# Optimization experiments

Hardware: AMD Instinct MI355X
Metric: run time of the kernel (lower is better)

Reference implementation:

```python
import jax, jax.numpy as jnp
import numpy as np

N_NODES = 50000
N_EDGES = 400000
N_GRAPHS = 64
D_IN = 256
D_HID = 256
D_OUT = 16


def _gcn_conv(x, edge_index, W, b):
    """PyG-style GCNConv: h = D^{-1/2}(A+I)D^{-1/2} (x @ W) + b."""
    n = x.shape[0]
    loop = jnp.arange(n)
    src = jnp.concatenate([edge_index[0], loop])  # [E+N]
    dst = jnp.concatenate([edge_index[1], loop])
    deg = jax.ops.segment_sum(jnp.ones_like(dst, x.dtype), dst, num_segments=n)
    dinv = jnp.where(deg > 0, jax.lax.rsqrt(deg), jnp.zeros_like(deg))
    norm = dinv[src] * dinv[dst]  # [E+N]
    h = x @ W  # linear transform first (as PyG does)
    msg = h[src] * norm[:, None]  # gather + scale, [E+N, D]
    out = jax.ops.segment_sum(msg, dst, num_segments=n)  # scatter-add
    return out + b


def setup_inputs() -> dict:
    key = jax.random.key(0)
    ks = jax.random.split(key, 12)
    x = jax.random.normal(ks[0], (N_NODES, D_IN), dtype=jnp.float32)
    edge_index = jax.random.randint(ks[1], (2, N_EDGES), 0, N_NODES, dtype=jnp.int64)
    batch = jnp.sort(jax.random.randint(ks[2], (N_NODES,), 0, N_GRAPHS, dtype=jnp.int64))

    def glorot(k, fan_in, fan_out):
        s = np.sqrt(6.0 / (fan_in + fan_out)).astype(np.float32)
        return jax.random.uniform(k, (fan_in, fan_out), jnp.float32, -s, s)

    return {
        "x": x,
        "edge_index": edge_index,
        "batch": batch,
        "W1": glorot(ks[3], D_IN, D_HID), "b1": jnp.zeros((D_HID,), jnp.float32),
        "W2": glorot(ks[4], D_HID, D_HID), "b2": jnp.zeros((D_HID,), jnp.float32),
        "W3": glorot(ks[5], D_HID, D_HID), "b3": jnp.zeros((D_HID,), jnp.float32),
        "Wfc": glorot(ks[6], D_HID, D_OUT), "bfc": jnp.zeros((D_OUT,), jnp.float32),
    }


def reference(x, edge_index, batch, W1, b1, W2, b2, W3, b3, Wfc, bfc):
    h = jax.nn.relu(_gcn_conv(x, edge_index, W1, b1))
    h = jax.nn.relu(_gcn_conv(h, edge_index, W2, b2))
    h = jax.nn.relu(_gcn_conv(h, edge_index, W3, b3))
    # global_mean_pool over batch ids
    sums = jax.ops.segment_sum(h, batch, num_segments=N_GRAPHS)  # [G, D]
    cnts = jax.ops.segment_sum(jnp.ones_like(batch, h.dtype), batch, num_segments=N_GRAPHS)
    pooled = sums / jnp.maximum(cnts, 1.0)[:, None]
    return pooled @ Wfc + bfc  # [G, D_OUT]
```

## Files before the change

### kernel.cpp

```cpp
#include <hip/hip_runtime.h>

#define NN 50000
#define NE 400000
#define NG 64
#define D 256
#define DOUT 16

typedef __attribute__((ext_vector_type(8))) _Float16 f16x8;
typedef __attribute__((ext_vector_type(8))) unsigned short u16x8;
typedef __attribute__((ext_vector_type(4))) float f32x4;

__device__ __forceinline__ unsigned short f2h(float x) {
    union { _Float16 h; unsigned short u; } v;
    v.h = (_Float16)x;
    return v.u;
}
__device__ __forceinline__ float h2f(unsigned short u) {
    union { _Float16 h; unsigned short u; } v;
    v.u = u;
    return (float)v.h;
}


__global__ void k_init(int* __restrict__ cnt, float* __restrict__ pooled,
                       const int* __restrict__ batch, float* __restrict__ inv_cnt,
                       int n) {
    int i = blockIdx.x * 256 + threadIdx.x;
    if (i < n) cnt[i] = 0;
    if (i < NG * D) pooled[i] = 0.f;
    if (blockIdx.x == 0 && threadIdx.x < NG) {
        int g = threadIdx.x;
        int lo = 0, hi = n;
        while (lo < hi) { int mid = (lo + hi) >> 1; if (batch[mid] < g) lo = mid + 1; else hi = mid; }
        int start = lo;
        hi = n;
        while (lo < hi) { int mid = (lo + hi) >> 1; if (batch[mid] < g + 1) lo = mid + 1; else hi = mid; }
        inv_cnt[g] = 1.f / fmaxf((float)(lo - start), 1.f);
    }
}


__global__ void k_split_count(const float* __restrict__ x, unsigned short* __restrict__ ahi,
                              int total4, int xblocks,
                              const float* __restrict__ W1, short* __restrict__ w1h,
                              const float* __restrict__ W2, short* __restrict__ w2h,
                              const float* __restrict__ W3, short* __restrict__ w3h,
                              const int* __restrict__ eidx, int* __restrict__ cnt, int E) {
    int b = blockIdx.x;
    if (b < xblocks) {
        int i = b * 256 + threadIdx.x;
        if (i >= total4) return;
        float4 v = ((const float4*)x)[i];
        ushort4 h;
        h.x = f2h(v.x);
        h.y = f2h(v.y);
        h.z = f2h(v.z);
        h.w = f2h(v.w);
        ((ushort4*)ahi)[i] = h;
    } else if (b < xblocks + 3 * 256) {
        int wb = b - xblocks;
        int which = wb >> 8;
        int idx = (wb & 255) * 256 + threadIdx.x;
        int nn = idx >> 8, k = idx & 255;
        const float* W = (which == 0) ? W1 : (which == 1) ? W2 : W3;
        short* Wh = (which == 0) ? w1h : (which == 1) ? w2h : w3h;
        Wh[idx] = (short)f2h(W[k * 256 + nn]);
    } else {
        int e = (b - xblocks - 3 * 256) * 256 + threadIdx.x;
        if (e < E) atomicAdd(&cnt[eidx[E + e]], 1);
    }
}

__global__ void k_scan1(const int* __restrict__ cnt, int* __restrict__ excl,
                        int* __restrict__ bsums, float* __restrict__ dinv, int n) {
    __shared__ int sh[256];
    int tid = threadIdx.x;
    int base = blockIdx.x * 1024;
    int v[4]; int tsum = 0;
    for (int j = 0; j < 4; ++j) {
        int i = base + tid * 4 + j;
        v[j] = (i < n) ? cnt[i] : 0;
        if (i < n) dinv[i] = rsqrtf((float)(v[j] + 1));
        tsum += v[j];
    }
    sh[tid] = tsum; __syncthreads();
    for (int d = 1; d < 256; d <<= 1) {
        int t = (tid >= d) ? sh[tid - d] : 0;
        __syncthreads();
        sh[tid] += t;
        __syncthreads();
    }
    int run = sh[tid] - tsum;
    for (int j = 0; j < 4; ++j) {
        int i = base + tid * 4 + j;
        if (i < n) excl[i] = run;
        run += v[j];
    }
    if (tid == 255) bsums[blockIdx.x] = sh[255];
}

__global__ void k_scan3(int* __restrict__ row_ptr, const int* __restrict__ bsums,
                        int* __restrict__ cursor, int n, int E, int nb) {
    __shared__ int off_s;
    int chunk = (int)(blockIdx.x >> 2);
    if (threadIdx.x < 64) {
        int v = ((int)threadIdx.x < nb && (int)threadIdx.x < chunk) ? bsums[threadIdx.x] : 0;
        #pragma unroll
        for (int d = 1; d < 64; d <<= 1) v += __shfl_xor(v, d);
        if (threadIdx.x == 0) off_s = v;
    }
    __syncthreads();
    int off = off_s;
    int i = blockIdx.x * 256 + threadIdx.x;
    if (i < n) {
        int v = row_ptr[i] + off;
        row_ptr[i] = v;
        cursor[i] = v;
    }
    if (i == 0) row_ptr[n] = E;
}


__device__ __forceinline__ void gemm_body(
        const unsigned short* __restrict__ A,
        const short* __restrict__ Wh,
        const float* __restrict__ dinv, unsigned short* __restrict__ C, int M,
        int bm) {
    const int tid = threadIdx.x;
    const int lane = tid & 63;
    const int w    = tid >> 6;
    const int lm   = lane & 15;
    const int quad = lane >> 4;

    const unsigned short* pa[4];
    const short* pb[4];
    #pragma unroll
    for (int i = 0; i < 4; ++i) {
        int ra = bm + i * 16 + lm; if (ra >= M) ra = M - 1;
        pa[i] = A + ((size_t)ra << 8) + quad * 8;
        int cb = w * 64 + i * 16 + lm;
        pb[i] = Wh + ((size_t)cb << 8) + quad * 8;
    }

    f32x4 acc[4][4];
    #pragma unroll
    for (int i = 0; i < 4; ++i)
        #pragma unroll
        for (int j = 0; j < 4; ++j)
            acc[i][j] = (f32x4){0.f, 0.f, 0.f, 0.f};

    #pragma unroll
    for (int k0 = 0; k0 < D; k0 += 32) {
        f16x8 Ah[4], Bh[4];
        #pragma unroll
        for (int i = 0; i < 4; ++i) {
            Ah[i] = *(const f16x8*)(pa[i] + k0);
            Bh[i] = *(const f16x8*)(pb[i] + k0);
        }
        #pragma unroll
        for (int mi = 0; mi < 4; ++mi)
            #pragma unroll
            for (int ni = 0; ni < 4; ++ni)
                acc[mi][ni] = __builtin_amdgcn_mfma_f32_16x16x32_f16(Ah[mi], Bh[ni], acc[mi][ni], 0, 0, 0);
    }

    #pragma unroll
    for (int mi = 0; mi < 4; ++mi) {
        int rbase = bm + mi * 16 + quad * 4;
        #pragma unroll
        for (int r = 0; r < 4; ++r) {
            int grow = rbase + r;
            if (grow < M) {
                float s = dinv[grow];
                #pragma unroll
                for (int ni = 0; ni < 4; ++ni) {
                    int col = w * 64 + ni * 16 + lm;
                    C[(size_t)grow * D + col] = f2h(acc[mi][ni][r] * s);
                }
            }
        }
    }
}

__global__ __launch_bounds__(256, 3) void k_gemm_mfma(
        const unsigned short* __restrict__ A,
        const short* __restrict__ Wh,
        const float* __restrict__ dinv, unsigned short* __restrict__ C, int M) {
    gemm_body(A, Wh, dinv, C, M, blockIdx.x * 64);
}

__global__ __launch_bounds__(256, 3) void k_gemm1_fill(
        const unsigned short* __restrict__ A,
        const short* __restrict__ Wh,
        const float* __restrict__ dinv, unsigned short* __restrict__ C, int M,
        int gblocks, const int* __restrict__ eidx, int* __restrict__ cursor,
        int* __restrict__ col_src, int E) {
    if ((int)blockIdx.x < gblocks) {
        gemm_body(A, Wh, dinv, C, M, blockIdx.x * 64);
    } else {
        int e = ((int)blockIdx.x - gblocks) * 256 + threadIdx.x;
        if (e < E) {
            int d = eidx[E + e];
            int pos = atomicAdd(&cursor[d], 1);
            col_src[pos] = eidx[e];
        }
    }
}


__global__ __launch_bounds__(256) void k_agg(
        const unsigned short* __restrict__ h, const float* __restrict__ dinv,
        const int* __restrict__ row_ptr, const int* __restrict__ col_src,
        const float* __restrict__ bias,
        unsigned short* __restrict__ ohi, int n) {
    int w = threadIdx.x >> 6, lane = threadIdx.x & 63;
    int node = blockIdx.x * 4 + w;
    if (node >= n) return;
    int half = lane >> 5;
    int dcol = lane & 31;

    float acc[8] = {0.f, 0.f, 0.f, 0.f, 0.f, 0.f, 0.f, 0.f};
    if (half == 0) {
        u16x8 sv = ((const u16x8*)(h + (size_t)node * D))[dcol];
        #pragma unroll
        for (int d = 0; d < 8; ++d) acc[d] = h2f(sv[d]);
    }

    int beg = row_ptr[node], end = row_ptr[node + 1];
    for (int c = beg; c < end; c += 64) {
        int cnt = min(64, end - c);
        int myidx = (lane < cnt) ? col_src[c + lane] : 0;
        for (int e = 0; e < cnt; e += 16) {
            u16x8 u[8];
            bool val[8];
            #pragma unroll
            for (int j = 0; j < 8; ++j) {
                int eid = e + j * 2 + half;
                val[j] = eid < cnt;
                if (val[j]) {
                    int s = __shfl(myidx, eid);
                    u[j] = ((const u16x8*)(h + (size_t)s * D))[dcol];
                }
            }
            #pragma unroll
            for (int j = 0; j < 8; ++j)
                if (val[j]) {
                    #pragma unroll
                    for (int d = 0; d < 8; ++d) acc[d] += h2f(u[j][d]);
                }
        }
    }

    #pragma unroll
    for (int d = 0; d < 8; ++d) acc[d] += __shfl_xor(acc[d], 32);

    if (half == 0) {
        float di = dinv[node];
        float4 b0 = ((const float4*)bias)[dcol * 2];
        float4 b1 = ((const float4*)bias)[dcol * 2 + 1];
        float bb[8] = {b0.x, b0.y, b0.z, b0.w, b1.x, b1.y, b1.z, b1.w};
        u16x8 o;
        #pragma unroll
        for (int d = 0; d < 8; ++d)
            o[d] = f2h(fmaxf(acc[d] * di + bb[d], 0.f));
        ((u16x8*)(ohi + (size_t)node * D))[dcol] = o;
    }
}


__global__ __launch_bounds__(256) void k_pool_sum(
        const unsigned short* __restrict__ hi,
        const int* __restrict__ batch, float* __restrict__ pooled, int n) {
    int beg = blockIdx.x * 64;
    if (beg >= n) return;
    int end = min(beg + 64, n);
    int t = threadIdx.x;
    float acc = 0.f;
    int cur = batch[beg];
    for (int i = beg; i < end; ++i) {
        int g = batch[i];
        if (g != cur) {
            atomicAdd(&pooled[cur * D + t], acc);
            acc = 0.f;
            cur = g;
        }
        acc += h2f(hi[(size_t)i * D + t]);
    }
    atomicAdd(&pooled[cur * D + t], acc);
}


__global__ void k_fc(const float* __restrict__ pooled, const float* __restrict__ inv_cnt,
                     const float* __restrict__ W, const float* __restrict__ b,
                     float* __restrict__ out) {
    int t = blockIdx.x * blockDim.x + threadIdx.x;
    if (t >= NG * DOUT) return;
    int g = t >> 4, o = t & 15;
    float acc = 0.f;
    for (int k = 0; k < D; ++k) acc += pooled[g * D + k] * W[k * DOUT + o];
    out[t] = acc * inv_cnt[g] + b[o];
}


extern "C" void kernel_launch(void* const* d_in, const int* in_sizes, int n_in,
                              void* d_out, int out_size, void* d_ws, size_t ws_size,
                              hipStream_t stream) {
    const float* x    = (const float*)d_in[0];
    const int*   eidx = (const int*)d_in[1];
    const int*   batch= (const int*)d_in[2];
    const float* W1   = (const float*)d_in[3];
    const float* b1   = (const float*)d_in[4];
    const float* W2   = (const float*)d_in[5];
    const float* b2   = (const float*)d_in[6];
    const float* W3   = (const float*)d_in[7];
    const float* b3   = (const float*)d_in[8];
    const float* Wfc  = (const float*)d_in[9];
    const float* bfc  = (const float*)d_in[10];
    float* out = (float*)d_out;

    const int n = in_sizes[0] / D;
    const int E = in_sizes[1] / 2;

    char* p = (char*)d_ws;
    auto take = [&](size_t bytes) -> void* {
        void* q = (void*)p;
        p += (bytes + 255) & ~(size_t)255;
        return q;
    };
    int*   cnt     = (int*)take((size_t)n * 4);
    int*   row_ptr = (int*)take((size_t)(n + 1) * 4);
    int*   cursor  = (int*)take((size_t)n * 4);
    int*   col_src = (int*)take((size_t)E * 4);
    int*   bsums   = (int*)take(256 * 4);
    float* dinv    = (float*)take((size_t)n * 4);
    float* inv_cnt = (float*)take((size_t)NG * 4);
    short* w1h     = (short*)take((size_t)D * D * 2);
    short* w2h     = (short*)take((size_t)D * D * 2);
    short* w3h     = (short*)take((size_t)D * D * 2);
    unsigned short* hbuf = (unsigned short*)take((size_t)n * D * 2);
    unsigned short* ahi  = (unsigned short*)take((size_t)n * D * 2);
    float* pooled  = (float*)take((size_t)NG * D * 4);

    int tb = 256;
    int gn = (n + tb - 1) / tb;
    int ge = (E + tb - 1) / tb;
    int nb = (n + 1023) / 1024;
    int total4 = n * D / 4;
    int xblocks = (total4 + 255) / 256;

    k_init<<<gn, tb, 0, stream>>>(cnt, pooled, batch, inv_cnt, n);
    k_split_count<<<xblocks + 3 * 256 + ge, tb, 0, stream>>>(
        x, ahi, total4, xblocks,
        W1, w1h, W2, w2h, W3, w3h,
        eidx, cnt, E);
    k_scan1<<<nb, 256, 0, stream>>>(cnt, row_ptr, bsums, dinv, n);
    k_scan3<<<gn, tb, 0, stream>>>(row_ptr, bsums, cursor, n, E, nb);

    int ggrid = (n + 63) / 64;
    int agrid = (n + 3) / 4;

    k_gemm1_fill<<<ggrid + ge, 256, 0, stream>>>(ahi, w1h, dinv, hbuf, n,
                                                 ggrid, eidx, cursor, col_src, E);
    k_agg<<<agrid, 256, 0, stream>>>(hbuf, dinv, row_ptr, col_src, b1, ahi, n);

    k_gemm_mfma<<<ggrid, 256, 0, stream>>>(ahi, w2h, dinv, hbuf, n);
    k_agg<<<agrid, 256, 0, stream>>>(hbuf, dinv, row_ptr, col_src, b2, ahi, n);

    k_gemm_mfma<<<ggrid, 256, 0, stream>>>(ahi, w3h, dinv, hbuf, n);
    k_agg<<<agrid, 256, 0, stream>>>(hbuf, dinv, row_ptr, col_src, b3, ahi, n);

    k_pool_sum<<<(n + 63) / 64, 256, 0, stream>>>(ahi, batch, pooled, n);
    k_fc<<<4, 256, 0, stream>>>(pooled, inv_cnt, Wfc, bfc, out);
}
```

Measured before the change: 400.7 us.

## Stage GEMM A tile in LDS via async global-to-LDS copies with swizzle

```diff
diff --git a/kernel.cpp b/kernel.cpp
--- a/kernel.cpp
+++ b/kernel.cpp
@@ -19,6 +19,12 @@
     union { _Float16 h; unsigned short u; } v;
     v.u = u;
     return (float)v.h;
+}
+
+__device__ __forceinline__ void async_cp16(void* lds, const void* g) {
+    __builtin_amdgcn_global_load_lds(
+        (const __attribute__((address_space(1))) unsigned int*)g,
+        (__attribute__((address_space(3))) unsigned int*)lds, 16, 0, 0);
 }
 
 
@@ -125,19 +131,28 @@
         const unsigned short* __restrict__ A,
         const short* __restrict__ Wh,
         const float* __restrict__ dinv, unsigned short* __restrict__ C, int M,
-        int bm) {
+        int bm, short* A_s) {
     const int tid = threadIdx.x;
     const int lane = tid & 63;
     const int w    = tid >> 6;
     const int lm   = lane & 15;
     const int quad = lane >> 4;
 
-    const unsigned short* pa[4];
+    {
+        const int sr = tid >> 5;
+        const int sc = tid & 31;
+        #pragma unroll
+        for (int j = 0; j < 8; ++j) {
+            int r = j * 8 + sr;
+            int ga = bm + r; if (ga >= M) ga = M - 1;
+            int q = sc ^ (r & 31);
+            async_cp16(&A_s[j * 2048 + w * 512], A + ((size_t)ga << 8) + q * 8);
+        }
+    }
+
     const short* pb[4];
     #pragma unroll
     for (int i = 0; i < 4; ++i) {
-        int ra = bm + i * 16 + lm; if (ra >= M) ra = M - 1;
-        pa[i] = A + ((size_t)ra << 8) + quad * 8;
         int cb = w * 64 + i * 16 + lm;
         pb[i] = Wh + ((size_t)cb << 8) + quad * 8;
     }
@@ -149,19 +164,35 @@
         for (int j = 0; j < 4; ++j)
             acc[i][j] = (f32x4){0.f, 0.f, 0.f, 0.f};
 
-    #pragma unroll
-    for (int k0 = 0; k0 < D; k0 += 32) {
-        f16x8 Ah[4], Bh[4];
-        #pragma unroll
-        for (int i = 0; i < 4; ++i) {
-            Ah[i] = *(const f16x8*)(pa[i] + k0);
-            Bh[i] = *(const f16x8*)(pb[i] + k0);
+    __syncthreads();
+
+    f16x8 Acur[4], Bcur[4], Anxt[4], Bnxt[4];
+    #pragma unroll
+    for (int i = 0; i < 4; ++i) {
+        int ra = i * 16 + lm;
+        Acur[i] = *(const f16x8*)&A_s[ra * 256 + (((quad) ^ (ra & 31)) << 3)];
+        Bcur[i] = *(const f16x8*)(pb[i]);
+    }
+
+    #pragma unroll
+    for (int ks = 0; ks < 8; ++ks) {
+        if (ks < 7) {
+            #pragma unroll
+            for (int i = 0; i < 4; ++i) {
+                int ra = i * 16 + lm;
+                Anxt[i] = *(const f16x8*)&A_s[ra * 256 + ((((ks + 1) * 4 + quad) ^ (ra & 31)) << 3)];
+                Bnxt[i] = *(const f16x8*)(pb[i] + (ks + 1) * 32);
+            }
         }
         #pragma unroll
         for (int mi = 0; mi < 4; ++mi)
             #pragma unroll
             for (int ni = 0; ni < 4; ++ni)
-                acc[mi][ni] = __builtin_amdgcn_mfma_f32_16x16x32_f16(Ah[mi], Bh[ni], acc[mi][ni], 0, 0, 0);
+                acc[mi][ni] = __builtin_amdgcn_mfma_f32_16x16x32_f16(Acur[mi], Bcur[ni], acc[mi][ni], 0, 0, 0);
+        if (ks < 7) {
+            #pragma unroll
+            for (int i = 0; i < 4; ++i) { Acur[i] = Anxt[i]; Bcur[i] = Bnxt[i]; }
+        }
     }
 
     #pragma unroll
@@ -186,7 +217,8 @@
         const unsigned short* __restrict__ A,
         const short* __restrict__ Wh,
         const float* __restrict__ dinv, unsigned short* __restrict__ C, int M) {
-    gemm_body(A, Wh, dinv, C, M, blockIdx.x * 64);
+    __shared__ short A_s[16384];
+    gemm_body(A, Wh, dinv, C, M, blockIdx.x * 64, A_s);
 }
 
 __global__ __launch_bounds__(256, 3) void k_gemm1_fill(
@@ -195,8 +227,9 @@
         const float* __restrict__ dinv, unsigned short* __restrict__ C, int M,
         int gblocks, const int* __restrict__ eidx, int* __restrict__ cursor,
         int* __restrict__ col_src, int E) {
+    __shared__ short A_s[16384];
     if ((int)blockIdx.x < gblocks) {
-        gemm_body(A, Wh, dinv, C, M, blockIdx.x * 64);
+        gemm_body(A, Wh, dinv, C, M, blockIdx.x * 64, A_s);
     } else {
         int e = ((int)blockIdx.x - gblocks) * 256 + threadIdx.x;
         if (e < E) {
```

Measured after the change: 367.7 us. 1.09x faster.
